# Performance work log

Hardware: AMD Instinct MI355X
Metric: run time of the kernel (lower is better)

Reference implementation:

```python
import jax, jax.numpy as jnp
import numpy as np

NEG_INF = -1.0e9
LEAKY_SLOPE = 0.2


def setup_inputs() -> dict:
    key = jax.random.key(0)
    k_h, k_w, k_wb, k_a, k_ab, k_m = jax.random.split(key, 6)
    B, S, N, F_in, F_out = 4, 256, 128, 128, 128
    h = jax.random.normal(k_h, (B, S, N, F_in), dtype=jnp.float32)
    # Linear(in_features, out_features): W_w [F_in, F_out], W_b [F_out]
    lim_w = 1.0 / np.sqrt(F_in)
    W_w = jax.random.uniform(k_w, (F_in, F_out), jnp.float32, -lim_w, lim_w)
    W_b = jax.random.uniform(k_wb, (F_out,), jnp.float32, -lim_w, lim_w)
    # Linear(2*F_out, 1): split the weight into a1 (acts on Wh_i) and a2 (acts on Wh_j)
    lim_a = 1.0 / np.sqrt(2 * F_out)
    a_full = jax.random.uniform(k_a, (2 * F_out,), jnp.float32, -lim_a, lim_a)
    a1, a2 = a_full[:F_out], a_full[F_out:]
    a_b = jax.random.uniform(k_ab, (), jnp.float32, -lim_a, lim_a)
    adj_mask = jax.random.randint(k_m, (N, N), 0, 2, dtype=jnp.int32)
    return {"h": h, "W_w": W_w, "W_b": W_b, "a1": a1, "a2": a2,
            "a_b": a_b, "adj_mask": adj_mask}


def reference(h, W_w, W_b, a1, a2, a_b, adj_mask):
    # h: [B, S, N, F_in]
    Wh = jnp.einsum('bsnf,fg->bsng', h, W_w) + W_b          # [B,S,N,F_out]
    # e_ij = leakyrelu(a . [Wh_i ; Wh_j] + b) = leakyrelu(f1_i + f2_j + b)
    f1 = jnp.einsum('bsng,g->bsn', Wh, a1)                   # row term
    f2 = jnp.einsum('bsng,g->bsn', Wh, a2)                   # col term
    e = jax.nn.leaky_relu(f1[..., :, None] + f2[..., None, :] + a_b,
                          negative_slope=LEAKY_SLOPE)        # [B,S,N,N]
    e = jnp.where(adj_mask == 0, NEG_INF, e)
    attention = jax.nn.softmax(e, axis=-1)
    # dropout is identity in eval mode (deterministic reference)
    h_prime = jnp.einsum('bsij,bsjg->bsig', attention, Wh)   # [B,S,N,F_out]
    return jax.nn.elu(h_prime)
```

## Files before the change

kernel.cpp:

```cpp
#include <hip/hip_runtime.h>
#include <hip/hip_bf16.h>
#include <cmath>

namespace {

typedef __attribute__((ext_vector_type(8))) short bf16x8;
typedef __attribute__((ext_vector_type(4))) float f32x4;

constexpr float kNegInf = -1000000000.0f;
constexpr float kSlope  = 0.2f;
constexpr float kLog2e  = 1.44269504088896340736f;

__device__ __forceinline__ unsigned short f2bf(float x) {
  unsigned int u = __float_as_uint(x);
  u = (u + 0x7FFFu + ((u >> 16) & 1u)) >> 16;
  return (unsigned short)u;
}
__device__ __forceinline__ unsigned int f2bf2(float a, float b) {
  __hip_bfloat162 t = __float22bfloat162_rn(float2{a, b});
  union { __hip_bfloat162 h; unsigned int u; } c;
  c.h = t;
  return c.u;
}
__device__ __forceinline__ float exp2_hw(float x) {
#if __has_builtin(__builtin_amdgcn_exp2f)
  return __builtin_amdgcn_exp2f(x);
#else
  float r;
  asm("v_exp_f32 %0, %1\n\ts_nop 1" : "=v"(r) : "v"(x));
  return r;
#endif
}


__global__ void prep(const float* __restrict__ Ww, const float* __restrict__ Wb,
                     const float* __restrict__ a1v, const float* __restrict__ a2v,
                     const int* __restrict__ adj,
                     unsigned short* __restrict__ wf, unsigned int* __restrict__ adjp,
                     float* __restrict__ ba) {
  const int tid = blockIdx.x * 256 + threadIdx.x;
  {
    const int j = tid & 7, l = (tid >> 3) & 63, kc = (tid >> 9) & 3, g = tid >> 11;
    const int k = kc * 32 + ((l >> 4) << 3) + j;
    const int c = l & 15;
    float x = 0.f;
    if (g < 8) {
      x = Ww[k * 128 + g * 16 + c];
    } else if (c < 2) {
      const float* av = (c == 0) ? a1v : a2v;
      float s = 0.f;
      for (int q = 0; q < 32; ++q) {
        f32x4 wv = *(const f32x4*)(Ww + k * 128 + q * 4);
        f32x4 aa = *(const f32x4*)(av + q * 4);
        s = fmaf(wv[0], aa[0], fmaf(wv[1], aa[1], fmaf(wv[2], aa[2], fmaf(wv[3], aa[3], s))));
      }
      x = s * kLog2e;
    }
    wf[tid] = f2bf(x);
  }
  if (tid < 512) {
    const int row = tid >> 2, wd = tid & 3;
    const int* ap = adj + row * 128 + wd * 32;
    unsigned int bits = 0u;
#pragma unroll
    for (int b = 0; b < 32; ++b) bits |= (ap[b] != 0 ? (1u << b) : 0u);
    adjp[tid] = bits;
  }
  if (tid >= 18368) {
    const int l = tid - 18368;
    float p1 = Wb[l] * a1v[l] + Wb[l + 64] * a1v[l + 64];
    float p2 = Wb[l] * a2v[l] + Wb[l + 64] * a2v[l + 64];
#pragma unroll
    for (int m = 1; m < 64; m <<= 1) {
      p1 += __shfl_xor(p1, m);
      p2 += __shfl_xor(p2, m);
    }
    if (l == 0) {
      ba[0] = p1 * kLog2e;
      ba[1] = p2 * kLog2e;
    }
  }
}

struct SMem {
  unsigned short wfs[9][4][64][8];
  union {
    struct {
      unsigned short Whs[8][4][64][8];
      float f1s[128];
      float f2s[128];
    } a;
    float stage[4][16][132];
  } u;
  unsigned int adjs[512];
};

__global__ __launch_bounds__(256, 2) void gat_fused3(
    const float* __restrict__ h,
    const float* __restrict__ Wb,
    const float* __restrict__ abp,
    const unsigned short* __restrict__ wf,
    const unsigned int* __restrict__ adjp,
    const float* __restrict__ ba,
    float* __restrict__ out,
    int BS) {
  __shared__ SMem sm;
  const int t    = threadIdx.x;
  const int lane = t & 63;
  const int w    = t >> 6;
  const int lr   = lane & 15;
  const int lg   = lane >> 4;
  const int R0   = w * 32;
  const float ab2 = abp[0] * kLog2e;
  const float ba1 = ba[0], ba2v = ba[1];

  float wbc[8];
#pragma unroll
  for (int g = 0; g < 8; ++g) wbc[g] = Wb[g * 16 + lr];

  constexpr int NB = 2;
  const int bs0 = blockIdx.x * NB;

  f32x4 wtmp[9];
  {
    const f32x4* wfg = (const f32x4*)wf;
#pragma unroll
    for (int p = 0; p < 9; ++p) wtmp[p] = wfg[p * 256 + t];
  }
  const uint2 adjv = *(const uint2*)(adjp + t * 2);

  f32x4 pre[16];
  {
    const float* hb = h + (size_t)bs0 * 16384;
#pragma unroll
    for (int rt = 0; rt < 2; ++rt)
#pragma unroll
      for (int kc = 0; kc < 4; ++kc) {
        const float* p = hb + (R0 + rt * 16 + lr) * 128 + kc * 32 + lg * 8;
        pre[(rt * 4 + kc) * 2]     = *(const f32x4*)p;
        pre[(rt * 4 + kc) * 2 + 1] = *(const f32x4*)(p + 4);
      }
  }

  {
    f32x4* wfl = (f32x4*)sm.wfs;
#pragma unroll
    for (int p = 0; p < 9; ++p) wfl[p * 256 + t] = wtmp[p];
    *(uint2*)(sm.adjs + t * 2) = adjv;
  }
  __syncthreads();

#pragma unroll
  for (int it = 0; it < NB; ++it) {
    const int bs = bs0 + it;
    if (bs >= BS) break;

    bf16x8 ha[2][4];
#pragma unroll
    for (int rt = 0; rt < 2; ++rt)
#pragma unroll
      for (int kc = 0; kc < 4; ++kc) {
        const f32x4 v0 = pre[(rt * 4 + kc) * 2];
        const f32x4 v1 = pre[(rt * 4 + kc) * 2 + 1];
        union { bf16x8 v; unsigned int u[4]; } pk;
        pk.u[0] = f2bf2(v0[0], v0[1]);
        pk.u[1] = f2bf2(v0[2], v0[3]);
        pk.u[2] = f2bf2(v1[0], v1[1]);
        pk.u[3] = f2bf2(v1[2], v1[3]);
        ha[rt][kc] = pk.v;
      }

    if (it + 1 < NB && bs + 1 < BS) {
      const float* hb = h + (size_t)(bs + 1) * 16384;
#pragma unroll
      for (int rt = 0; rt < 2; ++rt)
#pragma unroll
        for (int kc = 0; kc < 4; ++kc) {
          const float* p = hb + (R0 + rt * 16 + lr) * 128 + kc * 32 + lg * 8;
          pre[(rt * 4 + kc) * 2]     = *(const f32x4*)p;
          pre[(rt * 4 + kc) * 2 + 1] = *(const f32x4*)(p + 4);
        }
      __builtin_amdgcn_sched_barrier(0);
    }

    f32x4 acc[2][9];
#pragma unroll
    for (int rt = 0; rt < 2; ++rt)
#pragma unroll
      for (int g = 0; g < 9; ++g) acc[rt][g] = (f32x4){0.f, 0.f, 0.f, 0.f};

#pragma unroll
    for (int g = 0; g < 9; ++g)
#pragma unroll
      for (int kc = 0; kc < 4; ++kc) {
        const bf16x8 bh = *(const bf16x8*)(&sm.wfs[g][kc][lane][0]);
        acc[0][g] = __builtin_amdgcn_mfma_f32_16x16x32_bf16(ha[0][kc], bh, acc[0][g], 0, 0, 0);
        acc[1][g] = __builtin_amdgcn_mfma_f32_16x16x32_bf16(ha[1][kc], bh, acc[1][g], 0, 0, 0);
      }

    __syncthreads();

#pragma unroll
    for (int rt = 0; rt < 2; ++rt) {
#pragma unroll
      for (int r = 0; r < 4; ++r) {
#pragma unroll
        for (int g = 0; g < 8; ++g) acc[rt][g][r] += wbc[g];
        const int row = R0 + rt * 16 + lg * 4 + r;
        if (lr == 0)      sm.u.a.f1s[row] = acc[rt][8][r] + ba1;
        else if (lr == 1) sm.u.a.f2s[row] = acc[rt][8][r] + ba2v;
      }
#pragma unroll
      for (int g = 0; g < 8; ++g) {
        const unsigned int plo = f2bf2(acc[rt][g][0], acc[rt][g][1]);
        const unsigned int phi = f2bf2(acc[rt][g][2], acc[rt][g][3]);
        const int lp = (2 * rt + (lg >> 1)) * 16 + lr;
        const int jb = (lg & 1) * 4;
        *(uint2*)(&sm.u.a.Whs[g][w][lp][jb]) = make_uint2(plo, phi);
      }
    }
    __syncthreads();

    bf16x8 af[2][4];
    float s0 = 0.f, s1 = 0.f;
    const float f1i0 = sm.u.a.f1s[R0 + lr] + ab2;
    const float f1i1 = sm.u.a.f1s[R0 + 16 + lr] + ab2;
    const int rq0 = (R0 + lr) * 4, rq1 = (R0 + 16 + lr) * 4;
#pragma unroll
    for (int kc = 0; kc < 4; ++kc) {
      const f32x4 fv0 = *(const f32x4*)(&sm.u.a.f2s[kc * 32 + lg * 8]);
      const f32x4 fv1 = *(const f32x4*)(&sm.u.a.f2s[kc * 32 + lg * 8 + 4]);
      const unsigned int aw0 = sm.adjs[rq0 + kc];
      const unsigned int aw1 = sm.adjs[rq1 + kc];
      union { bf16x8 v; unsigned int u[4]; } pk0, pk1;
#pragma unroll
      for (int qq = 0; qq < 4; ++qq) {
        float e0[2], e1[2];
#pragma unroll
        for (int hh = 0; hh < 2; ++hh) {
          const int q = qq * 2 + hh;
          const float fj = (q < 4) ? fv0[q] : fv1[q - 4];
          const unsigned int bit = 1u << (lg * 8 + q);
          float x0 = f1i0 + fj;
          x0 = x0 >= 0.f ? x0 : kSlope * x0;
          x0 = (aw0 & bit) ? x0 : kNegInf;
          e0[hh] = exp2_hw(x0);
          float x1 = f1i1 + fj;
          x1 = x1 >= 0.f ? x1 : kSlope * x1;
          x1 = (aw1 & bit) ? x1 : kNegInf;
          e1[hh] = exp2_hw(x1);
        }
        const unsigned int u0 = f2bf2(e0[0], e0[1]);
        const unsigned int u1 = f2bf2(e1[0], e1[1]);
        pk0.u[qq] = u0;
        pk1.u[qq] = u1;
        s0 += __uint_as_float(u0 << 16) + __uint_as_float(u0 & 0xffff0000u);
        s1 += __uint_as_float(u1 << 16) + __uint_as_float(u1 & 0xffff0000u);
      }
      af[0][kc] = pk0.v;
      af[1][kc] = pk1.v;
    }
    s0 += __shfl_xor(s0, 16);
    s0 += __shfl_xor(s0, 32);
    s1 += __shfl_xor(s1, 16);
    s1 += __shfl_xor(s1, 32);
    float rs[2] = {s0, s1};

    f32x4 acc2[2][8];
#pragma unroll
    for (int rt = 0; rt < 2; ++rt)
#pragma unroll
      for (int g = 0; g < 8; ++g) acc2[rt][g] = (f32x4){0.f, 0.f, 0.f, 0.f};

#pragma unroll
    for (int g = 0; g < 8; ++g)
#pragma unroll
      for (int kc = 0; kc < 4; ++kc) {
        const bf16x8 bw = *(const bf16x8*)(&sm.u.a.Whs[g][kc][lane][0]);
        acc2[0][g] = __builtin_amdgcn_mfma_f32_16x16x32_bf16(af[0][kc], bw, acc2[0][g], 0, 0, 0);
        acc2[1][g] = __builtin_amdgcn_mfma_f32_16x16x32_bf16(af[1][kc], bw, acc2[1][g], 0, 0, 0);
      }
    __syncthreads();

    float* oblk = out + (size_t)bs * 16384;
#pragma unroll
    for (int rt = 0; rt < 2; ++rt) {
      float inv[4];
#pragma unroll
      for (int r = 0; r < 4; ++r) {
        const float lsum = __shfl(rs[rt], (lane & 48) | (lg * 4 + r));
        inv[r] = __builtin_amdgcn_rcpf(lsum);
      }
#pragma unroll
      for (int r = 0; r < 4; ++r)
#pragma unroll
        for (int g = 0; g < 8; ++g) {
          float v = acc2[rt][g][r] * inv[r];
          v = v > 0.f ? v : __expf(v) - 1.0f;
          sm.u.stage[w][lg * 4 + r][g * 16 + lr] = v;
        }
#pragma unroll
      for (int sstep = 0; sstep < 8; ++sstep) {
        const int row16 = ((sstep & 1) << 3) + (lane >> 3);
        const int cd    = ((sstep >> 1) << 5) + ((lane & 7) << 2);
        f32x4 vv = *(const f32x4*)(&sm.u.stage[w][row16][cd]);
        *(f32x4*)(oblk + (size_t)(R0 + rt * 16 + row16) * 128 + cd) = vv;
      }
    }
  }
}

}

extern "C" void kernel_launch(void* const* d_in, const int* in_sizes, int n_in,
                              void* d_out, int out_size, void* d_ws, size_t ws_size,
                              hipStream_t stream) {
  const float* h   = (const float*)d_in[0];
  const float* Ww  = (const float*)d_in[1];
  const float* Wb  = (const float*)d_in[2];
  const float* a1v = (const float*)d_in[3];
  const float* a2v = (const float*)d_in[4];
  const float* ab  = (const float*)d_in[5];
  const int*   adj = (const int*)d_in[6];
  float* out = (float*)d_out;

  unsigned short* wf   = (unsigned short*)d_ws;
  unsigned int*   adjp = (unsigned int*)((char*)d_ws + 36864);
  float*          ba   = (float*)((char*)d_ws + 38912);

  hipLaunchKernelGGL(prep, dim3(72), dim3(256), 0, stream, Ww, Wb, a1v, a2v, adj, wf, adjp, ba);

  const int BS = in_sizes[0] / 16384;
  const int grid = (BS + 1) / 2;
  hipLaunchKernelGGL(gat_fused3, dim3(grid), dim3(256), 0, stream,
                     h, Wb, ab, wf, adjp, ba, out, BS);
}
```

Measured before the change: 48.59 us.

## Use one 512-thread block per graph with 16 rows per wave

Replaces the 256-thread kernel that processed two (b,s) graphs per block with 32 rows per wave by one 512-thread block per graph, where each of eight waves handles 16 rows. Weight fragments and adjacency bits are read straight from global memory (cache) instead of being staged in shared memory, which shrinks LDS use so more blocks fit per CU. The cross-iteration prefetch of h is dropped and the output store is restaged in 4-row chunks. Latency hiding now relies on occupancy rather than software prefetch, and every block rereads the weights from global memory.

```diff
diff --git a/kernel.cpp b/kernel.cpp
--- a/kernel.cpp
+++ b/kernel.cpp
@@ -82,231 +82,145 @@
   }
 }
 
-struct SMem {
-  unsigned short wfs[9][4][64][8];
-  union {
-    struct {
-      unsigned short Whs[8][4][64][8];
-      float f1s[128];
-      float f2s[128];
-    } a;
-    float stage[4][16][132];
-  } u;
-  unsigned int adjs[512];
+union SMemU {
+  struct {
+    unsigned short Whs[8][4][64][8];
+    float f1s[128];
+    float f2s[128];
+  } a;
+  float stage[8][4][132];
 };
 
-__global__ __launch_bounds__(256, 2) void gat_fused3(
+__global__ __launch_bounds__(512, 8) void gat_fused8(
     const float* __restrict__ h,
     const float* __restrict__ Wb,
     const float* __restrict__ abp,
     const unsigned short* __restrict__ wf,
     const unsigned int* __restrict__ adjp,
     const float* __restrict__ ba,
-    float* __restrict__ out,
-    int BS) {
-  __shared__ SMem sm;
+    float* __restrict__ out) {
+  __shared__ SMemU sm;
   const int t    = threadIdx.x;
   const int lane = t & 63;
   const int w    = t >> 6;
   const int lr   = lane & 15;
   const int lg   = lane >> 4;
-  const int R0   = w * 32;
+  const int R0   = w * 16;
+  const int bs   = blockIdx.x;
   const float ab2 = abp[0] * kLog2e;
   const float ba1 = ba[0], ba2v = ba[1];
 
+  const float* hblk = h + (size_t)bs * 16384;
+  bf16x8 ha[4];
+#pragma unroll
+  for (int kc = 0; kc < 4; ++kc) {
+    const float* p = hblk + (R0 + lr) * 128 + kc * 32 + lg * 8;
+    const f32x4 v0 = *(const f32x4*)p;
+    const f32x4 v1 = *(const f32x4*)(p + 4);
+    union { bf16x8 v; unsigned int u[4]; } pk;
+    pk.u[0] = f2bf2(v0[0], v0[1]);
+    pk.u[1] = f2bf2(v0[2], v0[3]);
+    pk.u[2] = f2bf2(v1[0], v1[1]);
+    pk.u[3] = f2bf2(v1[2], v1[3]);
+    ha[kc] = pk.v;
+  }
+
+  f32x4 acc[9];
+#pragma unroll
+  for (int g = 0; g < 9; ++g) acc[g] = (f32x4){0.f, 0.f, 0.f, 0.f};
+#pragma unroll
+  for (int g = 0; g < 9; ++g)
+#pragma unroll
+    for (int kc = 0; kc < 4; ++kc) {
+      const bf16x8 bh = *(const bf16x8*)(wf + ((g * 4 + kc) * 64 + lane) * 8);
+      acc[g] = __builtin_amdgcn_mfma_f32_16x16x32_bf16(ha[kc], bh, acc[g], 0, 0, 0);
+    }
+
   float wbc[8];
 #pragma unroll
   for (int g = 0; g < 8; ++g) wbc[g] = Wb[g * 16 + lr];
-
-  constexpr int NB = 2;
-  const int bs0 = blockIdx.x * NB;
-
-  f32x4 wtmp[9];
-  {
-    const f32x4* wfg = (const f32x4*)wf;
-#pragma unroll
-    for (int p = 0; p < 9; ++p) wtmp[p] = wfg[p * 256 + t];
-  }
-  const uint2 adjv = *(const uint2*)(adjp + t * 2);
-
-  f32x4 pre[16];
-  {
-    const float* hb = h + (size_t)bs0 * 16384;
-#pragma unroll
-    for (int rt = 0; rt < 2; ++rt)
-#pragma unroll
-      for (int kc = 0; kc < 4; ++kc) {
-        const float* p = hb + (R0 + rt * 16 + lr) * 128 + kc * 32 + lg * 8;
-        pre[(rt * 4 + kc) * 2]     = *(const f32x4*)p;
-        pre[(rt * 4 + kc) * 2 + 1] = *(const f32x4*)(p + 4);
+#pragma unroll
+  for (int r = 0; r < 4; ++r) {
+#pragma unroll
+    for (int g = 0; g < 8; ++g) acc[g][r] += wbc[g];
+    const int row = R0 + lg * 4 + r;
+    if (lr == 0)      sm.a.f1s[row] = acc[8][r] + ba1;
+    else if (lr == 1) sm.a.f2s[row] = acc[8][r] + ba2v;
+  }
+#pragma unroll
+  for (int g = 0; g < 8; ++g) {
+    const unsigned int plo = f2bf2(acc[g][0], acc[g][1]);
+    const unsigned int phi = f2bf2(acc[g][2], acc[g][3]);
+    const int lp = (2 * (w & 1) + (lg >> 1)) * 16 + lr;
+    const int jb = (lg & 1) * 4;
+    *(uint2*)(&sm.a.Whs[g][w >> 1][lp][jb]) = make_uint2(plo, phi);
+  }
+  __syncthreads();
+
+  bf16x8 af[4];
+  float s0 = 0.f;
+  const float f1i = sm.a.f1s[R0 + lr] + ab2;
+  const int rq = (R0 + lr) * 4;
+#pragma unroll
+  for (int kc = 0; kc < 4; ++kc) {
+    const f32x4 fv0 = *(const f32x4*)(&sm.a.f2s[kc * 32 + lg * 8]);
+    const f32x4 fv1 = *(const f32x4*)(&sm.a.f2s[kc * 32 + lg * 8 + 4]);
+    const unsigned int aw = adjp[rq + kc];
+    union { bf16x8 v; unsigned int u[4]; } pk;
+#pragma unroll
+    for (int qq = 0; qq < 4; ++qq) {
+      float e[2];
+#pragma unroll
+      for (int hh = 0; hh < 2; ++hh) {
+        const int q = qq * 2 + hh;
+        const float fj = (q < 4) ? fv0[q] : fv1[q - 4];
+        float x = f1i + fj;
+        x = x >= 0.f ? x : kSlope * x;
+        x = ((aw >> (lg * 8 + q)) & 1u) ? x : kNegInf;
+        e[hh] = exp2_hw(x);
       }
-  }
-
-  {
-    f32x4* wfl = (f32x4*)sm.wfs;
-#pragma unroll
-    for (int p = 0; p < 9; ++p) wfl[p * 256 + t] = wtmp[p];
-    *(uint2*)(sm.adjs + t * 2) = adjv;
-  }
+      const unsigned int uu = f2bf2(e[0], e[1]);
+      pk.u[qq] = uu;
+      s0 += __uint_as_float(uu << 16) + __uint_as_float(uu & 0xffff0000u);
+    }
+    af[kc] = pk.v;
+  }
+  s0 += __shfl_xor(s0, 16);
+  s0 += __shfl_xor(s0, 32);
+
+  f32x4 acc2[8];
+#pragma unroll
+  for (int g = 0; g < 8; ++g) acc2[g] = (f32x4){0.f, 0.f, 0.f, 0.f};
+#pragma unroll
+  for (int g = 0; g < 8; ++g)
+#pragma unroll
+    for (int kc = 0; kc < 4; ++kc) {
+      const bf16x8 bw = *(const bf16x8*)(&sm.a.Whs[g][kc][lane][0]);
+      acc2[g] = __builtin_amdgcn_mfma_f32_16x16x32_bf16(af[kc], bw, acc2[g], 0, 0, 0);
+    }
   __syncthreads();
 
-#pragma unroll
-  for (int it = 0; it < NB; ++it) {
-    const int bs = bs0 + it;
-    if (bs >= BS) break;
-
-    bf16x8 ha[2][4];
-#pragma unroll
-    for (int rt = 0; rt < 2; ++rt)
-#pragma unroll
-      for (int kc = 0; kc < 4; ++kc) {
-        const f32x4 v0 = pre[(rt * 4 + kc) * 2];
-        const f32x4 v1 = pre[(rt * 4 + kc) * 2 + 1];
-        union { bf16x8 v; unsigned int u[4]; } pk;
-        pk.u[0] = f2bf2(v0[0], v0[1]);
-        pk.u[1] = f2bf2(v0[2], v0[3]);
-        pk.u[2] = f2bf2(v1[0], v1[1]);
-        pk.u[3] = f2bf2(v1[2], v1[3]);
-        ha[rt][kc] = pk.v;
-      }
-
-    if (it + 1 < NB && bs + 1 < BS) {
-      const float* hb = h + (size_t)(bs + 1) * 16384;
-#pragma unroll
-      for (int rt = 0; rt < 2; ++rt)
-#pragma unroll
-        for (int kc = 0; kc < 4; ++kc) {
-          const float* p = hb + (R0 + rt * 16 + lr) * 128 + kc * 32 + lg * 8;
-          pre[(rt * 4 + kc) * 2]     = *(const f32x4*)p;
-          pre[(rt * 4 + kc) * 2 + 1] = *(const f32x4*)(p + 4);
-        }
-      __builtin_amdgcn_sched_barrier(0);
-    }
-
-    f32x4 acc[2][9];
-#pragma unroll
-    for (int rt = 0; rt < 2; ++rt)
-#pragma unroll
-      for (int g = 0; g < 9; ++g) acc[rt][g] = (f32x4){0.f, 0.f, 0.f, 0.f};
-
-#pragma unroll
-    for (int g = 0; g < 9; ++g)
-#pragma unroll
-      for (int kc = 0; kc < 4; ++kc) {
-        const bf16x8 bh = *(const bf16x8*)(&sm.wfs[g][kc][lane][0]);
-        acc[0][g] = __builtin_amdgcn_mfma_f32_16x16x32_bf16(ha[0][kc], bh, acc[0][g], 0, 0, 0);
-        acc[1][g] = __builtin_amdgcn_mfma_f32_16x16x32_bf16(ha[1][kc], bh, acc[1][g], 0, 0, 0);
-      }
-
-    __syncthreads();
-
-#pragma unroll
-    for (int rt = 0; rt < 2; ++rt) {
-#pragma unroll
-      for (int r = 0; r < 4; ++r) {
-#pragma unroll
-        for (int g = 0; g < 8; ++g) acc[rt][g][r] += wbc[g];
-        const int row = R0 + rt * 16 + lg * 4 + r;
-        if (lr == 0)      sm.u.a.f1s[row] = acc[rt][8][r] + ba1;
-        else if (lr == 1) sm.u.a.f2s[row] = acc[rt][8][r] + ba2v;
-      }
-#pragma unroll
-      for (int g = 0; g < 8; ++g) {
-        const unsigned int plo = f2bf2(acc[rt][g][0], acc[rt][g][1]);
-        const unsigned int phi = f2bf2(acc[rt][g][2], acc[rt][g][3]);
-        const int lp = (2 * rt + (lg >> 1)) * 16 + lr;
-        const int jb = (lg & 1) * 4;
-        *(uint2*)(&sm.u.a.Whs[g][w][lp][jb]) = make_uint2(plo, phi);
-      }
-    }
-    __syncthreads();
-
-    bf16x8 af[2][4];
-    float s0 = 0.f, s1 = 0.f;
-    const float f1i0 = sm.u.a.f1s[R0 + lr] + ab2;
-    const float f1i1 = sm.u.a.f1s[R0 + 16 + lr] + ab2;
-    const int rq0 = (R0 + lr) * 4, rq1 = (R0 + 16 + lr) * 4;
-#pragma unroll
-    for (int kc = 0; kc < 4; ++kc) {
-      const f32x4 fv0 = *(const f32x4*)(&sm.u.a.f2s[kc * 32 + lg * 8]);
-      const f32x4 fv1 = *(const f32x4*)(&sm.u.a.f2s[kc * 32 + lg * 8 + 4]);
-      const unsigned int aw0 = sm.adjs[rq0 + kc];
-      const unsigned int aw1 = sm.adjs[rq1 + kc];
-      union { bf16x8 v; unsigned int u[4]; } pk0, pk1;
-#pragma unroll
-      for (int qq = 0; qq < 4; ++qq) {
-        float e0[2], e1[2];
-#pragma unroll
-        for (int hh = 0; hh < 2; ++hh) {
-          const int q = qq * 2 + hh;
-          const float fj = (q < 4) ? fv0[q] : fv1[q - 4];
-          const unsigned int bit = 1u << (lg * 8 + q);
-          float x0 = f1i0 + fj;
-          x0 = x0 >= 0.f ? x0 : kSlope * x0;
-          x0 = (aw0 & bit) ? x0 : kNegInf;
-          e0[hh] = exp2_hw(x0);
-          float x1 = f1i1 + fj;
-          x1 = x1 >= 0.f ? x1 : kSlope * x1;
-          x1 = (aw1 & bit) ? x1 : kNegInf;
-          e1[hh] = exp2_hw(x1);
-        }
-        const unsigned int u0 = f2bf2(e0[0], e0[1]);
-        const unsigned int u1 = f2bf2(e1[0], e1[1]);
-        pk0.u[qq] = u0;
-        pk1.u[qq] = u1;
-        s0 += __uint_as_float(u0 << 16) + __uint_as_float(u0 & 0xffff0000u);
-        s1 += __uint_as_float(u1 << 16) + __uint_as_float(u1 & 0xffff0000u);
-      }
-      af[0][kc] = pk0.v;
-      af[1][kc] = pk1.v;
-    }
-    s0 += __shfl_xor(s0, 16);
-    s0 += __shfl_xor(s0, 32);
-    s1 += __shfl_xor(s1, 16);
-    s1 += __shfl_xor(s1, 32);
-    float rs[2] = {s0, s1};
-
-    f32x4 acc2[2][8];
-#pragma unroll
-    for (int rt = 0; rt < 2; ++rt)
-#pragma unroll
-      for (int g = 0; g < 8; ++g) acc2[rt][g] = (f32x4){0.f, 0.f, 0.f, 0.f};
-
-#pragma unroll
-    for (int g = 0; g < 8; ++g)
-#pragma unroll
-      for (int kc = 0; kc < 4; ++kc) {
-        const bf16x8 bw = *(const bf16x8*)(&sm.u.a.Whs[g][kc][lane][0]);
-        acc2[0][g] = __builtin_amdgcn_mfma_f32_16x16x32_bf16(af[0][kc], bw, acc2[0][g], 0, 0, 0);
-        acc2[1][g] = __builtin_amdgcn_mfma_f32_16x16x32_bf16(af[1][kc], bw, acc2[1][g], 0, 0, 0);
-      }
-    __syncthreads();
-
-    float* oblk = out + (size_t)bs * 16384;
-#pragma unroll
-    for (int rt = 0; rt < 2; ++rt) {
-      float inv[4];
-#pragma unroll
-      for (int r = 0; r < 4; ++r) {
-        const float lsum = __shfl(rs[rt], (lane & 48) | (lg * 4 + r));
-        inv[r] = __builtin_amdgcn_rcpf(lsum);
-      }
-#pragma unroll
-      for (int r = 0; r < 4; ++r)
-#pragma unroll
-        for (int g = 0; g < 8; ++g) {
-          float v = acc2[rt][g][r] * inv[r];
-          v = v > 0.f ? v : __expf(v) - 1.0f;
-          sm.u.stage[w][lg * 4 + r][g * 16 + lr] = v;
-        }
-#pragma unroll
-      for (int sstep = 0; sstep < 8; ++sstep) {
-        const int row16 = ((sstep & 1) << 3) + (lane >> 3);
-        const int cd    = ((sstep >> 1) << 5) + ((lane & 7) << 2);
-        f32x4 vv = *(const f32x4*)(&sm.u.stage[w][row16][cd]);
-        *(f32x4*)(oblk + (size_t)(R0 + rt * 16 + row16) * 128 + cd) = vv;
-      }
-    }
+  float inv[4];
+#pragma unroll
+  for (int r = 0; r < 4; ++r) {
+    const float lsum = __shfl(s0, (lane & 48) | (lg * 4 + r));
+    inv[r] = __builtin_amdgcn_rcpf(lsum);
+  }
+  float* oblk = out + (size_t)bs * 16384;
+#pragma unroll
+  for (int p = 0; p < 4; ++p) {
+#pragma unroll
+    for (int g = 0; g < 8; ++g) {
+      float v = acc2[g][p] * inv[p];
+      v = v > 0.f ? v : __expf(v) - 1.0f;
+      sm.stage[w][lg][g * 16 + lr] = v;
+    }
+    const int col0 = (lane & 15) * 8;
+    const f32x4 v0 = *(const f32x4*)(&sm.stage[w][lane >> 4][col0]);
+    const f32x4 v1 = *(const f32x4*)(&sm.stage[w][lane >> 4][col0 + 4]);
+    float* orow = oblk + (size_t)(R0 + (lane >> 4) * 4 + p) * 128 + col0;
+    *(f32x4*)orow       = v0;
+    *(f32x4*)(orow + 4) = v1;
   }
 }
 
@@ -331,7 +245,6 @@
   hipLaunchKernelGGL(prep, dim3(72), dim3(256), 0, stream, Ww, Wb, a1v, a2v, adj, wf, adjp, ba);
 
   const int BS = in_sizes[0] / 16384;
-  const int grid = (BS + 1) / 2;
-  hipLaunchKernelGGL(gat_fused3, dim3(grid), dim3(256), 0, stream,
-                     h, Wb, ab, wf, adjp, ba, out, BS);
-}
+  hipLaunchKernelGGL(gat_fused8, dim3(BS), dim3(512), 0, stream,
+                     h, Wb, ab, wf, adjp, ba, out);
+}
```

After: 54.97 us. 1.13x slower.

## Process one graph per block, read weights and adjacency straight from global

Applied to the files above, without the earlier changes.

The kernel now handles a single (batch, seq) slice per block instead of two, which removes the software prefetch of the next slice's h tile and the loop around it. The weight fragments and adjacency bits are no longer staged in shared memory; weights are loaded per-lane from global (L2) inside the first MFMA loop, and each lane keeps its adjacency words in registers. This shrinks LDS and register use so launch bounds can ask for 4 blocks per SM, doubling the grid, at the cost of repeated global weight reads and losing the cross-slice load overlap.

```diff
diff --git a/kernel.cpp b/kernel.cpp
--- a/kernel.cpp
+++ b/kernel.cpp
@@ -82,230 +82,185 @@
   }
 }
 
-struct SMem {
-  unsigned short wfs[9][4][64][8];
-  union {
-    struct {
-      unsigned short Whs[8][4][64][8];
-      float f1s[128];
-      float f2s[128];
-    } a;
-    float stage[4][16][132];
-  } u;
-  unsigned int adjs[512];
+union SMemU {
+  struct {
+    unsigned short Whs[8][4][64][8];
+    float f1s[128];
+    float f2s[128];
+  } a;
+  float stage[4][16][132];
 };
 
-__global__ __launch_bounds__(256, 2) void gat_fused3(
+__global__ __launch_bounds__(256, 4) void gat_mfma(
     const float* __restrict__ h,
     const float* __restrict__ Wb,
     const float* __restrict__ abp,
     const unsigned short* __restrict__ wf,
     const unsigned int* __restrict__ adjp,
     const float* __restrict__ ba,
-    float* __restrict__ out,
-    int BS) {
-  __shared__ SMem sm;
+    float* __restrict__ out) {
+  __shared__ SMemU sm;
   const int t    = threadIdx.x;
   const int lane = t & 63;
   const int w    = t >> 6;
   const int lr   = lane & 15;
   const int lg   = lane >> 4;
+  const int bs   = blockIdx.x;
   const int R0   = w * 32;
   const float ab2 = abp[0] * kLog2e;
   const float ba1 = ba[0], ba2v = ba[1];
 
+  unsigned int aw0q[4], aw1q[4];
+  {
+    const int rq0 = (R0 + lr) * 4, rq1 = (R0 + 16 + lr) * 4;
+#pragma unroll
+    for (int kc = 0; kc < 4; ++kc) {
+      aw0q[kc] = adjp[rq0 + kc];
+      aw1q[kc] = adjp[rq1 + kc];
+    }
+  }
+
+  const float* hblk = h + (size_t)bs * 16384;
+
+  bf16x8 ha[2][4];
+#pragma unroll
+  for (int rt = 0; rt < 2; ++rt)
+#pragma unroll
+    for (int kc = 0; kc < 4; ++kc) {
+      const float* p = hblk + (R0 + rt * 16 + lr) * 128 + kc * 32 + lg * 8;
+      f32x4 v0 = *(const f32x4*)p;
+      f32x4 v1 = *(const f32x4*)(p + 4);
+      union { bf16x8 v; unsigned int u[4]; } pk;
+      pk.u[0] = f2bf2(v0[0], v0[1]);
+      pk.u[1] = f2bf2(v0[2], v0[3]);
+      pk.u[2] = f2bf2(v1[0], v1[1]);
+      pk.u[3] = f2bf2(v1[2], v1[3]);
+      ha[rt][kc] = pk.v;
+    }
+
+  f32x4 acc[2][9];
+#pragma unroll
+  for (int rt = 0; rt < 2; ++rt)
+#pragma unroll
+    for (int g = 0; g < 9; ++g) acc[rt][g] = (f32x4){0.f, 0.f, 0.f, 0.f};
+
+#pragma unroll
+  for (int g = 0; g < 9; ++g)
+#pragma unroll
+    for (int kc = 0; kc < 4; ++kc) {
+      const bf16x8 bh = *(const bf16x8*)(wf + ((g * 4 + kc) * 64 + lane) * 8);
+      acc[0][g] = __builtin_amdgcn_mfma_f32_16x16x32_bf16(ha[0][kc], bh, acc[0][g], 0, 0, 0);
+      acc[1][g] = __builtin_amdgcn_mfma_f32_16x16x32_bf16(ha[1][kc], bh, acc[1][g], 0, 0, 0);
+    }
+
   float wbc[8];
 #pragma unroll
   for (int g = 0; g < 8; ++g) wbc[g] = Wb[g * 16 + lr];
 
-  constexpr int NB = 2;
-  const int bs0 = blockIdx.x * NB;
-
-  f32x4 wtmp[9];
-  {
-    const f32x4* wfg = (const f32x4*)wf;
-#pragma unroll
-    for (int p = 0; p < 9; ++p) wtmp[p] = wfg[p * 256 + t];
-  }
-  const uint2 adjv = *(const uint2*)(adjp + t * 2);
-
-  f32x4 pre[16];
-  {
-    const float* hb = h + (size_t)bs0 * 16384;
-#pragma unroll
-    for (int rt = 0; rt < 2; ++rt)
-#pragma unroll
-      for (int kc = 0; kc < 4; ++kc) {
-        const float* p = hb + (R0 + rt * 16 + lr) * 128 + kc * 32 + lg * 8;
-        pre[(rt * 4 + kc) * 2]     = *(const f32x4*)p;
-        pre[(rt * 4 + kc) * 2 + 1] = *(const f32x4*)(p + 4);
+#pragma unroll
+  for (int rt = 0; rt < 2; ++rt) {
+#pragma unroll
+    for (int r = 0; r < 4; ++r) {
+#pragma unroll
+      for (int g = 0; g < 8; ++g) acc[rt][g][r] += wbc[g];
+      const int row = R0 + rt * 16 + lg * 4 + r;
+      if (lr == 0)      sm.a.f1s[row] = acc[rt][8][r] + ba1;
+      else if (lr == 1) sm.a.f2s[row] = acc[rt][8][r] + ba2v;
+    }
+#pragma unroll
+    for (int g = 0; g < 8; ++g) {
+      const unsigned int plo = f2bf2(acc[rt][g][0], acc[rt][g][1]);
+      const unsigned int phi = f2bf2(acc[rt][g][2], acc[rt][g][3]);
+      const int lp = (2 * rt + (lg >> 1)) * 16 + lr;
+      const int jb = (lg & 1) * 4;
+      *(uint2*)(&sm.a.Whs[g][w][lp][jb]) = make_uint2(plo, phi);
+    }
+  }
+  __syncthreads();
+
+  bf16x8 af[2][4];
+  float s0 = 0.f, s1 = 0.f;
+  const float f1i0 = sm.a.f1s[R0 + lr] + ab2;
+  const float f1i1 = sm.a.f1s[R0 + 16 + lr] + ab2;
+#pragma unroll
+  for (int kc = 0; kc < 4; ++kc) {
+    const f32x4 fv0 = *(const f32x4*)(&sm.a.f2s[kc * 32 + lg * 8]);
+    const f32x4 fv1 = *(const f32x4*)(&sm.a.f2s[kc * 32 + lg * 8 + 4]);
+    const unsigned int aw0 = aw0q[kc];
+    const unsigned int aw1 = aw1q[kc];
+    union { bf16x8 v; unsigned int u[4]; } pk0, pk1;
+#pragma unroll
+    for (int qq = 0; qq < 4; ++qq) {
+      float e0[2], e1[2];
+#pragma unroll
+      for (int hh = 0; hh < 2; ++hh) {
+        const int q = qq * 2 + hh;
+        const float fj = (q < 4) ? fv0[q] : fv1[q - 4];
+        const unsigned int bit = 1u << (lg * 8 + q);
+        float x0 = f1i0 + fj;
+        x0 = x0 >= 0.f ? x0 : kSlope * x0;
+        x0 = (aw0 & bit) ? x0 : kNegInf;
+        e0[hh] = exp2_hw(x0);
+        float x1 = f1i1 + fj;
+        x1 = x1 >= 0.f ? x1 : kSlope * x1;
+        x1 = (aw1 & bit) ? x1 : kNegInf;
+        e1[hh] = exp2_hw(x1);
       }
-  }
-
-  {
-    f32x4* wfl = (f32x4*)sm.wfs;
-#pragma unroll
-    for (int p = 0; p < 9; ++p) wfl[p * 256 + t] = wtmp[p];
-    *(uint2*)(sm.adjs + t * 2) = adjv;
-  }
+      const unsigned int u0 = f2bf2(e0[0], e0[1]);
+      const unsigned int u1 = f2bf2(e1[0], e1[1]);
+      pk0.u[qq] = u0;
+      pk1.u[qq] = u1;
+      s0 += __uint_as_float(u0 << 16) + __uint_as_float(u0 & 0xffff0000u);
+      s1 += __uint_as_float(u1 << 16) + __uint_as_float(u1 & 0xffff0000u);
+    }
+    af[0][kc] = pk0.v;
+    af[1][kc] = pk1.v;
+  }
+  s0 += __shfl_xor(s0, 16);
+  s0 += __shfl_xor(s0, 32);
+  s1 += __shfl_xor(s1, 16);
+  s1 += __shfl_xor(s1, 32);
+  float rs[2] = {s0, s1};
+
+  f32x4 acc2[2][8];
+#pragma unroll
+  for (int rt = 0; rt < 2; ++rt)
+#pragma unroll
+    for (int g = 0; g < 8; ++g) acc2[rt][g] = (f32x4){0.f, 0.f, 0.f, 0.f};
+
+#pragma unroll
+  for (int g = 0; g < 8; ++g)
+#pragma unroll
+    for (int kc = 0; kc < 4; ++kc) {
+      const bf16x8 bw = *(const bf16x8*)(&sm.a.Whs[g][kc][lane][0]);
+      acc2[0][g] = __builtin_amdgcn_mfma_f32_16x16x32_bf16(af[0][kc], bw, acc2[0][g], 0, 0, 0);
+      acc2[1][g] = __builtin_amdgcn_mfma_f32_16x16x32_bf16(af[1][kc], bw, acc2[1][g], 0, 0, 0);
+    }
   __syncthreads();
 
-#pragma unroll
-  for (int it = 0; it < NB; ++it) {
-    const int bs = bs0 + it;
-    if (bs >= BS) break;
-
-    bf16x8 ha[2][4];
-#pragma unroll
-    for (int rt = 0; rt < 2; ++rt)
-#pragma unroll
-      for (int kc = 0; kc < 4; ++kc) {
-        const f32x4 v0 = pre[(rt * 4 + kc) * 2];
-        const f32x4 v1 = pre[(rt * 4 + kc) * 2 + 1];
-        union { bf16x8 v; unsigned int u[4]; } pk;
-        pk.u[0] = f2bf2(v0[0], v0[1]);
-        pk.u[1] = f2bf2(v0[2], v0[3]);
-        pk.u[2] = f2bf2(v1[0], v1[1]);
-        pk.u[3] = f2bf2(v1[2], v1[3]);
-        ha[rt][kc] = pk.v;
+  float* oblk = out + (size_t)bs * 16384;
+#pragma unroll
+  for (int rt = 0; rt < 2; ++rt) {
+    float inv[4];
+#pragma unroll
+    for (int r = 0; r < 4; ++r) {
+      const float lsum = __shfl(rs[rt], (lane & 48) | (lg * 4 + r));
+      inv[r] = __builtin_amdgcn_rcpf(lsum);
+    }
+#pragma unroll
+    for (int r = 0; r < 4; ++r)
+#pragma unroll
+      for (int g = 0; g < 8; ++g) {
+        float v = acc2[rt][g][r] * inv[r];
+        v = v > 0.f ? v : __expf(v) - 1.0f;
+        sm.stage[w][lg * 4 + r][g * 16 + lr] = v;
       }
-
-    if (it + 1 < NB && bs + 1 < BS) {
-      const float* hb = h + (size_t)(bs + 1) * 16384;
-#pragma unroll
-      for (int rt = 0; rt < 2; ++rt)
-#pragma unroll
-        for (int kc = 0; kc < 4; ++kc) {
-          const float* p = hb + (R0 + rt * 16 + lr) * 128 + kc * 32 + lg * 8;
-          pre[(rt * 4 + kc) * 2]     = *(const f32x4*)p;
-          pre[(rt * 4 + kc) * 2 + 1] = *(const f32x4*)(p + 4);
-        }
-      __builtin_amdgcn_sched_barrier(0);
-    }
-
-    f32x4 acc[2][9];
-#pragma unroll
-    for (int rt = 0; rt < 2; ++rt)
-#pragma unroll
-      for (int g = 0; g < 9; ++g) acc[rt][g] = (f32x4){0.f, 0.f, 0.f, 0.f};
-
-#pragma unroll
-    for (int g = 0; g < 9; ++g)
-#pragma unroll
-      for (int kc = 0; kc < 4; ++kc) {
-        const bf16x8 bh = *(const bf16x8*)(&sm.wfs[g][kc][lane][0]);
-        acc[0][g] = __builtin_amdgcn_mfma_f32_16x16x32_bf16(ha[0][kc], bh, acc[0][g], 0, 0, 0);
-        acc[1][g] = __builtin_amdgcn_mfma_f32_16x16x32_bf16(ha[1][kc], bh, acc[1][g], 0, 0, 0);
-      }
-
-    __syncthreads();
-
-#pragma unroll
-    for (int rt = 0; rt < 2; ++rt) {
-#pragma unroll
-      for (int r = 0; r < 4; ++r) {
-#pragma unroll
-        for (int g = 0; g < 8; ++g) acc[rt][g][r] += wbc[g];
-        const int row = R0 + rt * 16 + lg * 4 + r;
-        if (lr == 0)      sm.u.a.f1s[row] = acc[rt][8][r] + ba1;
-        else if (lr == 1) sm.u.a.f2s[row] = acc[rt][8][r] + ba2v;
-      }
-#pragma unroll
-      for (int g = 0; g < 8; ++g) {
-        const unsigned int plo = f2bf2(acc[rt][g][0], acc[rt][g][1]);
-        const unsigned int phi = f2bf2(acc[rt][g][2], acc[rt][g][3]);
-        const int lp = (2 * rt + (lg >> 1)) * 16 + lr;
-        const int jb = (lg & 1) * 4;
-        *(uint2*)(&sm.u.a.Whs[g][w][lp][jb]) = make_uint2(plo, phi);
-      }
-    }
-    __syncthreads();
-
-    bf16x8 af[2][4];
-    float s0 = 0.f, s1 = 0.f;
-    const float f1i0 = sm.u.a.f1s[R0 + lr] + ab2;
-    const float f1i1 = sm.u.a.f1s[R0 + 16 + lr] + ab2;
-    const int rq0 = (R0 + lr) * 4, rq1 = (R0 + 16 + lr) * 4;
-#pragma unroll
-    for (int kc = 0; kc < 4; ++kc) {
-      const f32x4 fv0 = *(const f32x4*)(&sm.u.a.f2s[kc * 32 + lg * 8]);
-      const f32x4 fv1 = *(const f32x4*)(&sm.u.a.f2s[kc * 32 + lg * 8 + 4]);
-      const unsigned int aw0 = sm.adjs[rq0 + kc];
-      const unsigned int aw1 = sm.adjs[rq1 + kc];
-      union { bf16x8 v; unsigned int u[4]; } pk0, pk1;
-#pragma unroll
-      for (int qq = 0; qq < 4; ++qq) {
-        float e0[2], e1[2];
-#pragma unroll
-        for (int hh = 0; hh < 2; ++hh) {
-          const int q = qq * 2 + hh;
-          const float fj = (q < 4) ? fv0[q] : fv1[q - 4];
-          const unsigned int bit = 1u << (lg * 8 + q);
-          float x0 = f1i0 + fj;
-          x0 = x0 >= 0.f ? x0 : kSlope * x0;
-          x0 = (aw0 & bit) ? x0 : kNegInf;
-          e0[hh] = exp2_hw(x0);
-          float x1 = f1i1 + fj;
-          x1 = x1 >= 0.f ? x1 : kSlope * x1;
-          x1 = (aw1 & bit) ? x1 : kNegInf;
-          e1[hh] = exp2_hw(x1);
-        }
-        const unsigned int u0 = f2bf2(e0[0], e0[1]);
-        const unsigned int u1 = f2bf2(e1[0], e1[1]);
-        pk0.u[qq] = u0;
-        pk1.u[qq] = u1;
-        s0 += __uint_as_float(u0 << 16) + __uint_as_float(u0 & 0xffff0000u);
-        s1 += __uint_as_float(u1 << 16) + __uint_as_float(u1 & 0xffff0000u);
-      }
-      af[0][kc] = pk0.v;
-      af[1][kc] = pk1.v;
-    }
-    s0 += __shfl_xor(s0, 16);
-    s0 += __shfl_xor(s0, 32);
-    s1 += __shfl_xor(s1, 16);
-    s1 += __shfl_xor(s1, 32);
-    float rs[2] = {s0, s1};
-
-    f32x4 acc2[2][8];
-#pragma unroll
-    for (int rt = 0; rt < 2; ++rt)
-#pragma unroll
-      for (int g = 0; g < 8; ++g) acc2[rt][g] = (f32x4){0.f, 0.f, 0.f, 0.f};
-
-#pragma unroll
-    for (int g = 0; g < 8; ++g)
-#pragma unroll
-      for (int kc = 0; kc < 4; ++kc) {
-        const bf16x8 bw = *(const bf16x8*)(&sm.u.a.Whs[g][kc][lane][0]);
-        acc2[0][g] = __builtin_amdgcn_mfma_f32_16x16x32_bf16(af[0][kc], bw, acc2[0][g], 0, 0, 0);
-        acc2[1][g] = __builtin_amdgcn_mfma_f32_16x16x32_bf16(af[1][kc], bw, acc2[1][g], 0, 0, 0);
-      }
-    __syncthreads();
-
-    float* oblk = out + (size_t)bs * 16384;
-#pragma unroll
-    for (int rt = 0; rt < 2; ++rt) {
-      float inv[4];
-#pragma unroll
-      for (int r = 0; r < 4; ++r) {
-        const float lsum = __shfl(rs[rt], (lane & 48) | (lg * 4 + r));
-        inv[r] = __builtin_amdgcn_rcpf(lsum);
-      }
-#pragma unroll
-      for (int r = 0; r < 4; ++r)
-#pragma unroll
-        for (int g = 0; g < 8; ++g) {
-          float v = acc2[rt][g][r] * inv[r];
-          v = v > 0.f ? v : __expf(v) - 1.0f;
-          sm.u.stage[w][lg * 4 + r][g * 16 + lr] = v;
-        }
-#pragma unroll
-      for (int sstep = 0; sstep < 8; ++sstep) {
-        const int row16 = ((sstep & 1) << 3) + (lane >> 3);
-        const int cd    = ((sstep >> 1) << 5) + ((lane & 7) << 2);
-        f32x4 vv = *(const f32x4*)(&sm.u.stage[w][row16][cd]);
-        *(f32x4*)(oblk + (size_t)(R0 + rt * 16 + row16) * 128 + cd) = vv;
-      }
+#pragma unroll
+    for (int sstep = 0; sstep < 8; ++sstep) {
+      const int row16 = ((sstep & 1) << 3) + (lane >> 3);
+      const int cd    = ((sstep >> 1) << 5) + ((lane & 7) << 2);
+      f32x4 vv = *(const f32x4*)(&sm.stage[w][row16][cd]);
+      *(f32x4*)(oblk + (size_t)(R0 + rt * 16 + row16) * 128 + cd) = vv;
     }
   }
 }
@@ -331,7 +286,6 @@
   hipLaunchKernelGGL(prep, dim3(72), dim3(256), 0, stream, Ww, Wb, a1v, a2v, adj, wf, adjp, ba);
 
   const int BS = in_sizes[0] / 16384;
-  const int grid = (BS + 1) / 2;
-  hipLaunchKernelGGL(gat_fused3, dim3(grid), dim3(256), 0, stream,
-                     h, Wb, ab, wf, adjp, ba, out, BS);
-}
+  hipLaunchKernelGGL(gat_mfma, dim3(BS), dim3(256), 0, stream,
+                     h, Wb, ab, wf, adjp, ba, out);
+}
```

After: 43.74 us. 1.11x faster.
